# Kernel tuning notes

Measured on AMD Instinct MI355X. Metric: run time of the kernel, lower is better.

## Reference

```python
import jax, jax.numpy as jnp
import numpy as np
from jax import lax

PERM = (0, 1, 4, 5, 2, 3)  # swap the two (H,W) spatial pairs
DN = ('NCHWXY', 'OIHWXY', 'NCHWXY')  # 4 spatial dims -> native 4D conv


def conv4d(x, w, b):
    # x: [B,Ci,S,S,S,S], w: [Co,Ci,k1,k1,k2,k2], 'SAME' padding as in ANCNet Conv4d
    y = lax.conv_general_dilated(x, w, window_strides=(1, 1, 1, 1),
                                 padding='SAME', dimension_numbers=DN)
    return y + b[None, :, None, None, None, None]


def setup_inputs() -> dict:
    key = jax.random.key(0)
    ks = jax.random.split(key, 10)
    B, S = 2, 25
    def w_init(k, shape):
        fan_in = shape[1] * np.prod(shape[2:])
        return jax.random.normal(k, shape, jnp.float32) * (1.0 / np.sqrt(fan_in))
    return {
        'x': jax.random.normal(ks[0], (B, 1, S, S, S, S), jnp.float32),
        'w0': w_init(ks[1], (8, 1, 3, 3, 5, 5)),   'b0': jnp.zeros((8,), jnp.float32),
        'w1': w_init(ks[2], (8, 1, 5, 5, 5, 5)),   'b1': jnp.zeros((8,), jnp.float32),
        'w2a': w_init(ks[3], (16, 16, 5, 5, 5, 5)), 'b2a': jnp.zeros((16,), jnp.float32),
        'w2b': w_init(ks[4], (1, 16, 5, 5, 5, 5)),  'b2b': jnp.zeros((1,), jnp.float32),
    }


def reference(x, w0, b0, w1, b1, w2a, b2a, w2b, b2b):
    relu = jax.nn.relu
    conv0 = lambda t: relu(conv4d(t, w0, b0))
    conv1 = lambda t: relu(conv4d(t, w1, b1))
    conv2 = lambda t: relu(conv4d(relu(conv4d(t, w2a, b2a)), w2b, b2b))
    sym = lambda f, t: f(t) + jnp.transpose(f(jnp.transpose(t, PERM)), PERM)
    x0 = sym(conv0, x)
    x1 = sym(conv1, x)
    h = jnp.concatenate((x0, x1), axis=1)  # [B,16,S,S,S,S]
    return sym(conv2, h)
```

## Files before the change

### kernel.cpp

```cpp
#include <hip/hip_runtime.h>

#define S 25
#define PLANE 625
#define VOL 390625
#define CLn 12500000
#define HREG 6728
#define LDSPAD 20224

typedef __attribute__((ext_vector_type(8))) short short8;
typedef __attribute__((ext_vector_type(4))) float f32x4;
typedef __attribute__((ext_vector_type(4))) unsigned short us4;
typedef __attribute__((ext_vector_type(4))) unsigned int u32x4;

__device__ __forceinline__ unsigned short f2bf(float f) {
    unsigned int u = __float_as_uint(f);
    u += 0x7fffu + ((u >> 16) & 1u);
    return (unsigned short)(u >> 16);
}

__device__ __forceinline__ int xcd_swz(int orig, int nwg) {
    int q = nwg >> 3, r = nwg & 7;
    int x = orig & 7, lid = orig >> 3;
    return (x < r ? x * (q + 1) : r * (q + 1) + (x - r) * q) + lid;
}

__device__ __forceinline__ int nxt_kd(int kd, int d0, int d1) {
    #pragma unroll 1
    for (++kd; kd < 25; ++kd) {
        int kd0 = kd / 5, kd1 = kd - kd0 * 5;
        int e0 = d0 + kd0 - 2, e1 = d1 + kd1 - 2;
        if (e0 >= 0 && e0 < S && e1 >= 0 && e1 < S) return kd;
    }
    return 25;
}

__device__ __forceinline__ int nxt_w(int uv, int U, int V, int b0, int b1) {
    #pragma unroll 1
    for (++uv; uv < U * V; ++uv) {
        int u = uv / V, v = uv - u * V;
        int e0 = b0 + u, e1 = b1 + v;
        if (e0 >= 0 && e0 < S && e1 >= 0 && e1 < S) return uv;
    }
    return U * V;
}

__global__ __launch_bounds__(256) void prep_weights(
    const float* __restrict__ w2a, const float* __restrict__ w2b,
    const float* __restrict__ w0, const float* __restrict__ w1,
    unsigned short* __restrict__ wbig, unsigned short* __restrict__ wl1,
    unsigned short* __restrict__ wcp)
{
    int idx = blockIdx.x * 256 + threadIdx.x;
    if (idx < 332800) {
        int k = idx & 31;
        int co = (idx >> 5) & 15;
        int tile = (idx >> 9) & 1;
        int rem = idx >> 10;
        int pr = rem % 13, kd01 = rem / 13;
        int t = 2 * pr + (k >> 4), ci = k & 15;
        float v = 0.f;
        if (t <= 24)
            v = (tile == 0) ? w2a[(co * 16 + ci) * 625 + kd01 * 25 + t]
                            : w2a[(co * 16 + ci) * 625 + t * 25 + kd01];
        wbig[idx] = f2bf(v);
    } else if (idx < 358400) {
        int j = idx - 332800;
        int k = j & 31;
        int row = (j >> 5) & 15;
        int tile = (j >> 9) & 1;
        int kd01 = j >> 10;
        int kd0 = kd01 / 5, kd1 = kd01 - kd0 * 5;
        float v = 0.f;
        if (k < 25) {
            int t = k, kd2 = t / 5, kd3 = t - kd2 * 5;
            if (tile == 0) {
                v = (row < 8) ? w1[row * 625 + kd0 * 125 + kd1 * 25 + t]
                              : w1[(row - 8) * 625 + t * 25 + kd01];
            } else {
                if (row < 8) {
                    if (kd0 >= 1 && kd0 <= 3 && kd1 >= 1 && kd1 <= 3)
                        v = w0[((row * 3 + (kd0 - 1)) * 3 + (kd1 - 1)) * 25 + t];
                } else {
                    if (kd2 >= 1 && kd2 <= 3 && kd3 >= 1 && kd3 <= 3)
                        v = w0[(row - 8) * 225 + ((kd2 - 1) * 3 + (kd3 - 1)) * 25 + kd01];
                }
            }
        }
        wl1[j] = f2bf(v);
    } else if (idx < 358400 + 614400) {
        int j = idx - 358400;
        int k = j & 31;
        int row = (j >> 5) & 15;
        int rem = j >> 9;
        int t = rem % 25, uv = rem / 25;
        int u = uv >> 3, v8 = uv & 7;
        int path = row & 1, o = row >> 1;
        int py = o >> 2, px = o & 3;
        int kd0 = u - py, kd1 = v8 - px;
        float v = 0.f;
        if (kd0 >= 0 && kd0 < 5 && kd1 >= 0 && kd1 < 5) {
            int ci = k & 15;
            if (path == 0 && k < 16)
                v = w2b[ci * 625 + (kd0 * 5 + kd1) * 25 + t];
            else if (path == 1 && k >= 16)
                v = w2b[ci * 625 + t * 25 + kd0 * 5 + kd1];
        }
        wcp[j] = f2bf(v);
    }
}

__global__ __launch_bounds__(256) void layer1_mfma(
    const float* __restrict__ x, const unsigned short* __restrict__ wl1,
    const float* __restrict__ b0, const float* __restrict__ b1,
    unsigned short* __restrict__ hbf)
{
    __shared__ __align__(16) unsigned short pl[29 * 32];
    const int blk = blockIdx.x;
    const int b = blk / PLANE;
    const int d01 = blk - b * PLANE;
    const int d0 = d01 / S, d1 = d01 - d0 * S;
    const int tid = threadIdx.x;
    const int l = tid & 63, w = tid >> 6;
    const int col = l & 15, kq = l >> 4;

    int off[8];
    #pragma unroll
    for (int j = 0; j < 8; ++j) {
        int t = kq * 8 + j; if (t > 24) t = 24;
        int t5 = t / 5;
        off[j] = t5 * 32 + (t - t5 * 5);
    }
    int rb[10];
    #pragma unroll
    for (int g = 0; g < 10; ++g) {
        int n = (w * 10 + g) * 16 + col; if (n > 624) n = 624;
        int d2 = n / 25;
        rb[g] = d2 * 32 + (n - d2 * 25);
    }

    f32x4 acc0[10], acc1[10];
    #pragma unroll
    for (int g = 0; g < 10; ++g) {
        acc0[g] = (f32x4){0.f, 0.f, 0.f, 0.f};
        acc1[g] = (f32x4){0.f, 0.f, 0.f, 0.f};
    }

    const float* xb = x + (size_t)b * VOL;

    #pragma unroll 1
    for (int kd01 = 0; kd01 < 25; ++kd01) {
        const int kd0 = kd01 / 5, kd1 = kd01 - kd0 * 5;
        const int e0 = d0 + kd0 - 2, e1 = d1 + kd1 - 2;
        if (e0 < 0 || e0 >= S || e1 < 0 || e1 >= S) continue;
        __syncthreads();
        {
            const float* sp = xb + (e0 * 25 + e1) * 625;
            for (int i = tid; i < 841; i += 256) {
                int r = i / 29, c = i - r * 29;
                float v = 0.f;
                if (r >= 2 && r <= 26 && c >= 2 && c <= 26)
                    v = sp[(r - 2) * 25 + (c - 2)];
                pl[r * 32 + c] = f2bf(v);
            }
        }
        __syncthreads();
        const unsigned short* wp = wl1 + kd01 * 1024;
        short8 a0 = *(const short8*)(wp + col * 32 + kq * 8);
        short8 a1 = *(const short8*)(wp + 512 + col * 32 + kq * 8);
        #pragma unroll
        for (int g = 0; g < 10; ++g) {
            short8 bf;
            #pragma unroll
            for (int j = 0; j < 8; ++j)
                bf[j] = (short)pl[rb[g] + off[j]];
            acc0[g] = __builtin_amdgcn_mfma_f32_16x16x32_bf16(a0, bf, acc0[g], 0, 0, 0);
            acc1[g] = __builtin_amdgcn_mfma_f32_16x16x32_bf16(a1, bf, acc1[g], 0, 0, 0);
        }
    }

    const int ch = (kq & 1) * 4;
    float bi1[4], bi0[4];
    #pragma unroll
    for (int r = 0; r < 4; ++r) { bi1[r] = b1[ch + r]; bi0[r] = b0[ch + r]; }
    const bool lo = (kq < 2);
    const size_t obase = (size_t)(b * 625 + d01) * 625;
    #pragma unroll
    for (int g = 0; g < 10; ++g) {
        int n = (w * 10 + g) * 16 + col;
        float r0[4], r1[4];
        #pragma unroll
        for (int r = 0; r < 4; ++r) {
            r0[r] = fmaxf(acc0[g][r] + bi1[r], 0.f);
            r1[r] = fmaxf(acc1[g][r] + bi0[r], 0.f);
        }
        us4 u0, u1;
        #pragma unroll
        for (int r = 0; r < 4; ++r) {
            float p0 = __shfl_xor(r0[r], 32, 64);
            float p1 = __shfl_xor(r1[r], 32, 64);
            u0[r] = f2bf(r0[r] + p0);
            u1[r] = f2bf(r1[r] + p1);
        }
        if (lo && n < 625) {
            *(us4*)&hbf[(obase + n) * 16 + 8 + ch] = u0;
            *(us4*)&hbf[(obase + n) * 16 + ch]     = u1;
        }
    }
}

__global__ __launch_bounds__(256, 3) void conv_mfma(
    const unsigned short* __restrict__ in, const unsigned short* __restrict__ wq,
    const float* __restrict__ bias,
    unsigned short* __restrict__ gA, unsigned short* __restrict__ gB)
{
    __shared__ __align__(16) unsigned short pl[LDSPAD];
    const int blk = xcd_swz(blockIdx.x, 1250);
    const int b = blk / PLANE;
    const int d01 = blk - b * PLANE;
    const int d0 = d01 / S, d1 = d01 - d0 * S;
    const int tid = threadIdx.x;
    const int l = tid & 63, w = tid >> 6;
    const int tp = l >> 5;
    const int kq = (l >> 4) & 3;
    const int col = l & 15;

    int ofsG[7], ofsL[7]; bool ok[7];
    #pragma unroll
    for (int j = 0; j < 7; ++j) {
        int cid = tid + j * 256;
        int h = (cid >= 841) ? 1 : 0;
        int pt = cid - h * 841;
        int r = pt / 29, c = pt - r * 29;
        ok[j] = (cid < 1682) && (r >= 2 && r <= 26 && c >= 2 && c <= 26);
        ofsG[j] = ((r - 2) * 25 + (c - 2)) * 16 + h * 8;
        ofsL[j] = h * HREG + pt * 8;
    }

    int rbo[10];
    #pragma unroll
    for (int g = 0; g < 10; ++g) {
        int n = (w * 10 + g) * 16 + col;
        if (n > 624) n = 624;
        int d2 = n / 25, d3 = n - d2 * 25;
        rbo[g] = (d2 * 29 + d3) * 8 + (kq & 1) * HREG;
    }

    f32x4 acc[10][2];
    #pragma unroll
    for (int g = 0; g < 10; ++g) {
        acc[g][0] = (f32x4){0.f, 0.f, 0.f, 0.f};
        acc[g][1] = (f32x4){0.f, 0.f, 0.f, 0.f};
    }

    const unsigned short* inb = in + (size_t)b * 6250000;

    u32x4 stg[7];
    int kd_cur = nxt_kd(-1, d0, d1);
    {
        int kd0 = kd_cur / 5, kd1 = kd_cur - kd0 * 5;
        const unsigned short* sb = inb + (size_t)((d0 + kd0 - 2) * 25 + (d1 + kd1 - 2)) * 10000;
        #pragma unroll
        for (int j = 0; j < 7; ++j) {
            u32x4 z = {0u, 0u, 0u, 0u};
            if (ok[j]) z = *(const u32x4*)(sb + ofsG[j]);
            stg[j] = z;
        }
    }

    #pragma unroll 1
    while (kd_cur < 25) {
        const int kd01 = kd_cur;
        const int kd_nxt = nxt_kd(kd_cur, d0, d1);
        __syncthreads();
        #pragma unroll
        for (int j = 0; j < 7; ++j)
            if (j < 6 || tid < 146) *(u32x4*)&pl[ofsL[j]] = stg[j];
        __syncthreads();
        if (kd_nxt < 25) {
            int kd0 = kd_nxt / 5, kd1 = kd_nxt - kd0 * 5;
            const unsigned short* sb = inb + (size_t)((d0 + kd0 - 2) * 25 + (d1 + kd1 - 2)) * 10000;
            #pragma unroll
            for (int j = 0; j < 7; ++j) {
                u32x4 z = {0u, 0u, 0u, 0u};
                if (ok[j]) z = *(const u32x4*)(sb + ofsG[j]);
                stg[j] = z;
            }
        }

        #pragma unroll 1
        for (int pr = 0; pr < 13; ++pr) {
            const unsigned short* wp = wq + (size_t)kd01 * 13312 + pr * 1024;
            short8 a0 = *(const short8*)(wp + col * 32 + kq * 8);
            short8 a1 = *(const short8*)(wp + 512 + col * 32 + kq * 8);
            int t = 2 * pr + tp;
            if (t > 24) t = 24;
            int t5 = t / 5;
            int toff8 = (t5 * 29 + (t - t5 * 5)) * 8;
            #pragma unroll
            for (int g = 0; g < 10; ++g) {
                short8 bfrag = *(const short8*)&pl[rbo[g] + toff8];
                acc[g][0] = __builtin_amdgcn_mfma_f32_16x16x32_bf16(a0, bfrag, acc[g][0], 0, 0, 0);
                acc[g][1] = __builtin_amdgcn_mfma_f32_16x16x32_bf16(a1, bfrag, acc[g][1], 0, 0, 0);
            }
        }
        kd_cur = kd_nxt;
    }

    const int cob = kq * 4;
    float bi[4];
    #pragma unroll
    for (int r = 0; r < 4; ++r) bi[r] = bias[cob + r];
    #pragma unroll
    for (int g = 0; g < 10; ++g) {
        int n = (w * 10 + g) * 16 + col;
        if (n < 625) {
            size_t ob = ((size_t)(b * 625 + d01) * 625 + n) * 16 + cob;
            us4 ua, ub;
            #pragma unroll
            for (int r = 0; r < 4; ++r) {
                ua[r] = f2bf(fmaxf(acc[g][0][r] + bi[r], 0.f));
                ub[r] = f2bf(fmaxf(acc[g][1][r] + bi[r], 0.f));
            }
            *(us4*)&gA[ob] = ua;
            *(us4*)&gB[ob] = ub;
        }
    }
}

__global__ __launch_bounds__(128, 2) void convc_v3(
    const unsigned short* __restrict__ gA,
    const unsigned short* __restrict__ wcp, const float* __restrict__ b2b,
    float* __restrict__ outp)
{
    __shared__ __align__(16) unsigned short pl[348 * 36];
    const int blk = xcd_swz(blockIdx.x, 728);
    const int q = blk & 3;
    const int geo = blk >> 2;
    const int b = geo / 91;
    const int g91 = geo - b * 91;
    const int t0 = g91 / 7, t1 = g91 - t0 * 7;
    const int D0 = t0 * 2, D1 = t1 * 4;
    const int r0 = (q == 0) ? -2 : (q == 1) ? 4 : (q == 2) ? 10 : 17;
    const int tid = threadIdx.x;
    const int l = tid & 63, w = tid >> 6;
    const int col = l & 15, kq = l >> 4;

    int ofsG[11], ofsL[11]; bool ok[11];
    #pragma unroll
    for (int j = 0; j < 11; ++j) {
        int cid = tid + j * 128;
        int p = cid >> 2, qq = cid & 3;
        int r = p / 29, c = p - r * 29;
        int d2e = r + r0, d3e = c - 2;
        ok[j] = (cid < 1392) && (d2e >= 0 && d2e < S) && (d3e >= 0 && d3e < S);
        ofsG[j] = (qq >> 1) * CLn + (d2e * 25 + d3e) * 16 + (qq & 1) * 8;
        ofsL[j] = p * 36 + qq * 8;
    }

    int rb[5];
    #pragma unroll
    for (int g = 0; g < 5; ++g) {
        int n = q * 160 + (w * 5 + g) * 16 + col; if (n > 624) n = 624;
        int d2 = n / 25;
        rb[g] = ((d2 - r0 - 2) * 29 + (n - d2 * 25)) * 36;
    }

    f32x4 acc[5];
    #pragma unroll
    for (int g = 0; g < 5; ++g) acc[g] = (f32x4){0.f, 0.f, 0.f, 0.f};

    const unsigned short* gAb = gA + (size_t)b * 6250000;

    u32x4 stg[11];
    int uv_cur = nxt_w(-1, 6, 8, D0 - 2, D1 - 2);
    {
        int u = uv_cur >> 3, v = uv_cur & 7;
        const unsigned short* sb = gAb + (size_t)((D0 - 2 + u) * 25 + (D1 - 2 + v)) * 10000;
        #pragma unroll
        for (int j = 0; j < 11; ++j) {
            u32x4 z = {0u, 0u, 0u, 0u};
            if (ok[j]) z = *(const u32x4*)(sb + ofsG[j]);
            stg[j] = z;
        }
    }

    #pragma unroll 1
    while (uv_cur < 48) {
        const int uvc = uv_cur;
        const int uv_nxt = nxt_w(uv_cur, 6, 8, D0 - 2, D1 - 2);
        __syncthreads();
        #pragma unroll
        for (int j = 0; j < 11; ++j)
            if (j < 10 || tid < 112) *(u32x4*)&pl[ofsL[j]] = stg[j];
        __syncthreads();
        if (uv_nxt < 48) {
            int u = uv_nxt >> 3, v = uv_nxt & 7;
            const unsigned short* sb = gAb + (size_t)((D0 - 2 + u) * 25 + (D1 - 2 + v)) * 10000;
            #pragma unroll
            for (int j = 0; j < 11; ++j) {
                u32x4 z = {0u, 0u, 0u, 0u};
                if (ok[j]) z = *(const u32x4*)(sb + ofsG[j]);
                stg[j] = z;
            }
        }

        const unsigned short* wbase = wcp + (size_t)uvc * 12800;
        #pragma unroll 1
        for (int t = 0; t < 25; ++t) {
            const int t5 = t / 5;
            const int toff = (t5 * 29 + (t - t5 * 5)) * 36;
            short8 a = *(const short8*)(wbase + (t * 16 + col) * 32 + kq * 8);
            #pragma unroll
            for (int g = 0; g < 5; ++g) {
                short8 bf = *(const short8*)&pl[rb[g] + toff + kq * 8];
                acc[g] = __builtin_amdgcn_mfma_f32_16x16x32_bf16(a, bf, acc[g], 0, 0, 0);
            }
        }
        uv_cur = uv_nxt;
    }

    const float bv = b2b[0];
    #pragma unroll
    for (int g = 0; g < 5; ++g) {
        int n = q * 160 + (w * 5 + g) * 16 + col;
        if (n < 625) {
            #pragma unroll
            for (int r2 = 0; r2 < 2; ++r2) {
                int o = kq * 2 + r2;
                int d0 = D0 + (o >> 2), d1 = D1 + (o & 3);
                if (d0 < S && d1 < S) {
                    float vA = acc[g][r2 * 2], vB = acc[g][r2 * 2 + 1];
                    outp[((size_t)b * 625 + d0 * 25 + d1) * 625 + n] =
                        fmaxf(vA + bv, 0.f) + fmaxf(vB + bv, 0.f);
                }
            }
        }
    }
}

extern "C" void kernel_launch(void* const* d_in, const int* in_sizes, int n_in,
                              void* d_out, int out_size, void* d_ws, size_t ws_size,
                              hipStream_t stream) {
    const float* x   = (const float*)d_in[0];
    const float* w0  = (const float*)d_in[1];
    const float* b0  = (const float*)d_in[2];
    const float* w1  = (const float*)d_in[3];
    const float* b1  = (const float*)d_in[4];
    const float* w2a = (const float*)d_in[5];
    const float* b2a = (const float*)d_in[6];
    const float* w2b = (const float*)d_in[7];
    const float* b2b = (const float*)d_in[8];
    float* out = (float*)d_out;

    unsigned short* hbf  = (unsigned short*)d_ws;
    unsigned short* gA   = hbf + CLn;
    unsigned short* gB   = gA + CLn;
    unsigned short* wbig = gB + CLn;
    unsigned short* wl1  = wbig + 332800;
    unsigned short* wcp  = wl1 + 25600;
    if (ws_size < ((size_t)3 * CLn + 332800 + 25600 + 614400) * sizeof(unsigned short)) return;

    prep_weights<<<3800, 256, 0, stream>>>(w2a, w2b, w0, w1, wbig, wl1, wcp);
    layer1_mfma<<<1250, 256, 0, stream>>>(x, wl1, b0, b1, hbf);
    conv_mfma<<<1250, 256, 0, stream>>>(hbf, wbig, b2a, gA, gB);
    convc_v3<<<728, 128, 0, stream>>>(gA, wcp, b2b, out);
}
```

Baseline: 962.0 us.

## Switch middle conv to 32x32x16 MFMA with both paths stacked in M

Rewrites the 16-to-16 channel conv kernel to use 32x32x16 bf16 MFMA instructions. The two symmetric paths (normal and transposed weights) are stacked as 32 output rows, and the K dimension is the 16 input channels per tap. The weight layout is repacked to match, and each wave now covers 5 groups of 32 spatial columns instead of 10 groups of 16. This removes the padded odd tap-pair and halves the number of LDS B-fragment reads per MFMA FLOP. In exchange it uses larger accumulator tiles (16 floats per group) and a more complex epilogue scatter.

```diff
diff --git a/kernel.cpp b/kernel.cpp
--- a/kernel.cpp
+++ b/kernel.cpp
@@ -9,6 +9,7 @@
 
 typedef __attribute__((ext_vector_type(8))) short short8;
 typedef __attribute__((ext_vector_type(4))) float f32x4;
+typedef __attribute__((ext_vector_type(16))) float f32x16;
 typedef __attribute__((ext_vector_type(4))) unsigned short us4;
 typedef __attribute__((ext_vector_type(4))) unsigned int u32x4;
 
@@ -47,24 +48,21 @@
 __global__ __launch_bounds__(256) void prep_weights(
     const float* __restrict__ w2a, const float* __restrict__ w2b,
     const float* __restrict__ w0, const float* __restrict__ w1,
-    unsigned short* __restrict__ wbig, unsigned short* __restrict__ wl1,
+    unsigned short* __restrict__ wbig32, unsigned short* __restrict__ wl1,
     unsigned short* __restrict__ wcp)
 {
     int idx = blockIdx.x * 256 + threadIdx.x;
-    if (idx < 332800) {
-        int k = idx & 31;
-        int co = (idx >> 5) & 15;
-        int tile = (idx >> 9) & 1;
-        int rem = idx >> 10;
-        int pr = rem % 13, kd01 = rem / 13;
-        int t = 2 * pr + (k >> 4), ci = k & 15;
-        float v = 0.f;
-        if (t <= 24)
-            v = (tile == 0) ? w2a[(co * 16 + ci) * 625 + kd01 * 25 + t]
-                            : w2a[(co * 16 + ci) * 625 + t * 25 + kd01];
-        wbig[idx] = f2bf(v);
-    } else if (idx < 358400) {
-        int j = idx - 332800;
+    if (idx < 320000) {
+        int k = idx & 15;
+        int m = (idx >> 4) & 31;
+        int rem = idx >> 9;
+        int t = rem % 25, kd01 = rem / 25;
+        float v;
+        if (m < 16) v = w2a[(m * 16 + k) * 625 + kd01 * 25 + t];
+        else        v = w2a[((m - 16) * 16 + k) * 625 + t * 25 + kd01];
+        wbig32[idx] = f2bf(v);
+    } else if (idx < 345600) {
+        int j = idx - 320000;
         int k = j & 31;
         int row = (j >> 5) & 15;
         int tile = (j >> 9) & 1;
@@ -87,8 +85,8 @@
             }
         }
         wl1[j] = f2bf(v);
-    } else if (idx < 358400 + 614400) {
-        int j = idx - 358400;
+    } else if (idx < 345600 + 614400) {
+        int j = idx - 345600;
         int k = j & 31;
         int row = (j >> 5) & 15;
         int rem = j >> 9;
@@ -208,7 +206,7 @@
     }
 }
 
-__global__ __launch_bounds__(256, 3) void conv_mfma(
+__global__ __launch_bounds__(256, 3) void conv_mfma32(
     const unsigned short* __restrict__ in, const unsigned short* __restrict__ wq,
     const float* __restrict__ bias,
     unsigned short* __restrict__ gA, unsigned short* __restrict__ gB)
@@ -220,37 +218,35 @@
     const int d0 = d01 / S, d1 = d01 - d0 * S;
     const int tid = threadIdx.x;
     const int l = tid & 63, w = tid >> 6;
-    const int tp = l >> 5;
-    const int kq = (l >> 4) & 3;
-    const int col = l & 15;
+    const int h = l >> 5;
+    const int nl = l & 31;
 
     int ofsG[7], ofsL[7]; bool ok[7];
     #pragma unroll
     for (int j = 0; j < 7; ++j) {
         int cid = tid + j * 256;
-        int h = (cid >= 841) ? 1 : 0;
-        int pt = cid - h * 841;
+        int hh = (cid >= 841) ? 1 : 0;
+        int pt = cid - hh * 841;
         int r = pt / 29, c = pt - r * 29;
         ok[j] = (cid < 1682) && (r >= 2 && r <= 26 && c >= 2 && c <= 26);
-        ofsG[j] = ((r - 2) * 25 + (c - 2)) * 16 + h * 8;
-        ofsL[j] = h * HREG + pt * 8;
-    }
-
-    int rbo[10];
-    #pragma unroll
-    for (int g = 0; g < 10; ++g) {
-        int n = (w * 10 + g) * 16 + col;
+        ofsG[j] = ((r - 2) * 25 + (c - 2)) * 16 + hh * 8;
+        ofsL[j] = hh * HREG + pt * 8;
+    }
+
+    int rbo[5];
+    #pragma unroll
+    for (int g = 0; g < 5; ++g) {
+        int n = (w * 5 + g) * 32 + nl;
         if (n > 624) n = 624;
         int d2 = n / 25, d3 = n - d2 * 25;
-        rbo[g] = (d2 * 29 + d3) * 8 + (kq & 1) * HREG;
-    }
-
-    f32x4 acc[10][2];
-    #pragma unroll
-    for (int g = 0; g < 10; ++g) {
-        acc[g][0] = (f32x4){0.f, 0.f, 0.f, 0.f};
-        acc[g][1] = (f32x4){0.f, 0.f, 0.f, 0.f};
-    }
+        rbo[g] = h * HREG + (d2 * 29 + d3) * 8;
+    }
+
+    f32x16 acc[5];
+    #pragma unroll
+    for (int g = 0; g < 5; ++g)
+        #pragma unroll
+        for (int r = 0; r < 16; ++r) acc[g][r] = 0.f;
 
     const unsigned short* inb = in + (size_t)b * 6250000;
 
@@ -287,42 +283,38 @@
             }
         }
 
+        const unsigned short* wkd = wq + (size_t)kd01 * 25 * 512 + nl * 16 + h * 8;
         #pragma unroll 1
-        for (int pr = 0; pr < 13; ++pr) {
-            const unsigned short* wp = wq + (size_t)kd01 * 13312 + pr * 1024;
-            short8 a0 = *(const short8*)(wp + col * 32 + kq * 8);
-            short8 a1 = *(const short8*)(wp + 512 + col * 32 + kq * 8);
-            int t = 2 * pr + tp;
-            if (t > 24) t = 24;
+        for (int t = 0; t < 25; ++t) {
+            short8 a = *(const short8*)(wkd + t * 512);
             int t5 = t / 5;
-            int toff8 = (t5 * 29 + (t - t5 * 5)) * 8;
-            #pragma unroll
-            for (int g = 0; g < 10; ++g) {
-                short8 bfrag = *(const short8*)&pl[rbo[g] + toff8];
-                acc[g][0] = __builtin_amdgcn_mfma_f32_16x16x32_bf16(a0, bfrag, acc[g][0], 0, 0, 0);
-                acc[g][1] = __builtin_amdgcn_mfma_f32_16x16x32_bf16(a1, bfrag, acc[g][1], 0, 0, 0);
+            int toff = (t5 * 29 + (t - t5 * 5)) * 8;
+            #pragma unroll
+            for (int g = 0; g < 5; ++g) {
+                short8 bf = *(const short8*)&pl[rbo[g] + toff];
+                acc[g] = __builtin_amdgcn_mfma_f32_32x32x16_bf16(a, bf, acc[g], 0, 0, 0);
             }
         }
         kd_cur = kd_nxt;
     }
 
-    const int cob = kq * 4;
-    float bi[4];
-    #pragma unroll
-    for (int r = 0; r < 4; ++r) bi[r] = bias[cob + r];
-    #pragma unroll
-    for (int g = 0; g < 10; ++g) {
-        int n = (w * 10 + g) * 16 + col;
+    #pragma unroll
+    for (int g = 0; g < 5; ++g) {
+        int n = (w * 5 + g) * 32 + nl;
         if (n < 625) {
-            size_t ob = ((size_t)(b * 625 + d01) * 625 + n) * 16 + cob;
-            us4 ua, ub;
-            #pragma unroll
-            for (int r = 0; r < 4; ++r) {
-                ua[r] = f2bf(fmaxf(acc[g][0][r] + bi[r], 0.f));
-                ub[r] = f2bf(fmaxf(acc[g][1][r] + bi[r], 0.f));
-            }
-            *(us4*)&gA[ob] = ua;
-            *(us4*)&gB[ob] = ub;
+            size_t ob = ((size_t)(b * 625 + d01) * 625 + n) * 16;
+            #pragma unroll
+            for (int q = 0; q < 4; ++q) {
+                int baserow = q * 8 + 4 * h;
+                us4 u;
+                #pragma unroll
+                for (int r = 0; r < 4; ++r) {
+                    int co = (baserow + r) & 15;
+                    u[r] = f2bf(fmaxf(acc[g][q * 4 + r] + bias[co], 0.f));
+                }
+                if (baserow < 16) *(us4*)&gA[ob + baserow] = u;
+                else              *(us4*)&gB[ob + baserow - 16] = u;
+            }
         }
     }
 }
@@ -452,16 +444,16 @@
     const float* b2b = (const float*)d_in[8];
     float* out = (float*)d_out;
 
-    unsigned short* hbf  = (unsigned short*)d_ws;
-    unsigned short* gA   = hbf + CLn;
-    unsigned short* gB   = gA + CLn;
-    unsigned short* wbig = gB + CLn;
-    unsigned short* wl1  = wbig + 332800;
-    unsigned short* wcp  = wl1 + 25600;
-    if (ws_size < ((size_t)3 * CLn + 332800 + 25600 + 614400) * sizeof(unsigned short)) return;
-
-    prep_weights<<<3800, 256, 0, stream>>>(w2a, w2b, w0, w1, wbig, wl1, wcp);
+    unsigned short* hbf    = (unsigned short*)d_ws;
+    unsigned short* gA     = hbf + CLn;
+    unsigned short* gB     = gA + CLn;
+    unsigned short* wbig32 = gB + CLn;
+    unsigned short* wl1    = wbig32 + 320000;
+    unsigned short* wcp    = wl1 + 25600;
+    if (ws_size < ((size_t)3 * CLn + 320000 + 25600 + 614400) * sizeof(unsigned short)) return;
+
+    prep_weights<<<3750, 256, 0, stream>>>(w2a, w2b, w0, w1, wbig32, wl1, wcp);
     layer1_mfma<<<1250, 256, 0, stream>>>(x, wl1, b0, b1, hbf);
-    conv_mfma<<<1250, 256, 0, stream>>>(hbf, wbig, b2a, gA, gB);
+    conv_mfma32<<<1250, 256, 0, stream>>>(hbf, wbig32, b2a, gA, gB);
     convc_v3<<<728, 128, 0, stream>>>(gA, wcp, b2b, out);
 }
```

Result: no change. 953.1 us (-0.9%).
